# Kernel optimization log

Hardware: AMD Instinct MI355X
Metric: run time of the kernel (lower is better)

## Reference

```python
import jax, jax.numpy as jnp
import numpy as np
import math

B, S, D, H, W = 1, 2048, 512, 8, 64
DK = D // H
NEG = -1e9


def setup_inputs() -> dict:
    rng = jax.random.key(0)
    ks = jax.random.split(rng, 8)
    sc = 0.02
    return {
        "query": jax.random.normal(ks[0], (B, S, D), jnp.float32),
        "key": jax.random.normal(ks[1], (B, S, D), jnp.float32),
        "value": jax.random.normal(ks[2], (B, S, D), jnp.float32),
        "Wq": jax.random.normal(ks[3], (D, D), jnp.float32) * sc,
        "Wk": jax.random.normal(ks[4], (D, D), jnp.float32) * sc,
        "Wv": jax.random.normal(ks[5], (D, D), jnp.float32) * sc,
        "Wo": jax.random.normal(ks[6], (D, D), jnp.float32) * sc,
        "bo": jax.random.normal(ks[7], (D,), jnp.float32) * sc,
    }


def reference(query, key, value, Wq, Wk, Wv, Wo, bo):
    b, s, d = query.shape

    def proj(x, Wm):
        # [B,S,D] -> [B,H,S,DK]
        return (x @ Wm.T).reshape(b, s, H, DK).transpose(0, 2, 1, 3)

    Q = proj(query, Wq)
    K = proj(key, Wk)
    V = proj(value, Wv)

    i = jnp.arange(s)
    rel = jnp.arange(-W, 1)                     # causal band: keys i-W..i
    idx = i[:, None] + rel[None, :]             # [S, W+1]
    valid = idx >= 0
    idxc = jnp.clip(idx, 0, s - 1)

    Kw = K[:, :, idxc, :]                       # [B,H,S,W+1,DK]
    Vw = V[:, :, idxc, :]

    scores = jnp.einsum('bhsd,bhsrd->bhsr', Q, Kw) / math.sqrt(DK)
    decay_bias = 0.1 * jnp.exp(-0.1 * jnp.abs(rel.astype(jnp.float32)))
    scores = jnp.where(valid[None, None], scores + decay_bias, NEG)
    probs = jax.nn.softmax(scores, axis=-1)     # [B,H,S,W+1]

    out = jnp.einsum('bhsr,bhsrd->bhsd', probs, Vw)
    out = out.transpose(0, 2, 1, 3).reshape(b, s, d)
    output = out @ Wo.T + bo

    # attention_weights [B,H,S,2W]: only rows with window_size <= 2W are written
    win = jnp.minimum(s, i + W + 1) - jnp.maximum(0, i - W)   # [S]
    stored = win <= 2 * W
    slot = jnp.arange(2 * W)
    ridx = slot[None, :] + jnp.maximum(W - i, 0)[:, None]     # [S,2W] slot->band index
    vmask = (ridx <= W) & (slot[None, :] < win[:, None]) & stored[:, None]
    gath = jnp.take_along_axis(probs, jnp.clip(ridx, 0, W)[None, None], axis=-1)
    attn_w = jnp.where(vmask[None, None], gath, 0.0)

    return output, attn_w
```

## Files before the change

kernel.cpp:

```cpp
#include <hip/hip_runtime.h>
#include <stdint.h>

#define SEQ   2048
#define DM    512
#define NHEAD 8
#define DKH   64
#define WIN   64
#define NEGV  -1000000000.0f

typedef __attribute__((ext_vector_type(8))) short          short8;
typedef __attribute__((ext_vector_type(4))) float          float4v;
typedef __attribute__((ext_vector_type(8))) unsigned short ushort8v;

__device__ __forceinline__ unsigned short f2bf(float x) {
    uint32_t u = __float_as_uint(x);
    uint32_t r = (u + 0x7FFFu + ((u >> 16) & 1u)) >> 16;
    return (unsigned short)r;
}
__device__ __forceinline__ float bf2f(unsigned short u) {
    return __uint_as_float(((uint32_t)u) << 16);
}

__device__ __forceinline__ void async_cp16(const void* g, void* lds) {
    __builtin_amdgcn_global_load_lds(
        (const __attribute__((address_space(1))) unsigned int*)(uintptr_t)g,
        (__attribute__((address_space(3))) unsigned int*)(uint32_t)(uintptr_t)lds,
        16, 0, 0);
}

__global__ __launch_bounds__(256)
void cast7_kernel(const float* __restrict__ q, const float* __restrict__ k,
                  const float* __restrict__ v, const float* __restrict__ wq,
                  const float* __restrict__ wk, const float* __restrict__ wv,
                  const float* __restrict__ wo, unsigned short* __restrict__ dst)
{
    int g = (blockIdx.x * 256 + threadIdx.x) * 8;
    const float* src; int off;
    if      (g < 1048576) { src = q;  off = g; }
    else if (g < 2097152) { src = k;  off = g - 1048576; }
    else if (g < 3145728) { src = v;  off = g - 2097152; }
    else if (g < 3407872) { src = wq; off = g - 3145728; }
    else if (g < 3670016) { src = wk; off = g - 3407872; }
    else if (g < 3932160) { src = wv; off = g - 3670016; }
    else                  { src = wo; off = g - 3932160; }
    float4 x0 = *(const float4*)(src + off);
    float4 x1 = *(const float4*)(src + off + 4);
    ushort8v o;
    o[0] = f2bf(x0.x); o[1] = f2bf(x0.y); o[2] = f2bf(x0.z); o[3] = f2bf(x0.w);
    o[4] = f2bf(x1.x); o[5] = f2bf(x1.y); o[6] = f2bf(x1.z); o[7] = f2bf(x1.w);
    *(ushort8v*)(dst + g) = o;
}

template<bool BIAS, bool OUT_BF16>
__device__ __forceinline__ void gemm_mfma_body(const unsigned short* __restrict__ A,
                                               const unsigned short* __restrict__ B,
                                               const float* __restrict__ bias,
                                               void* __restrict__ Cv)
{
    __shared__ __align__(16) unsigned short As[128 * 32];
    __shared__ __align__(16) unsigned short Bs[128 * 32];

    const int tid  = threadIdx.x;
    const int m0   = blockIdx.x * 128;
    const int n0   = blockIdx.y * 128;
    const int lane = tid & 63;
    const int wave = tid >> 6;
    const int wm   = (wave >> 1) * 64;
    const int wn   = (wave & 1) * 64;
    const int lm   = lane & 15;
    const int lk   = (lane >> 4) * 8;

    float4v acc[4][4] = {};

    for (int k0 = 0; k0 < 512; k0 += 32) {
        #pragma unroll
        for (int h = 0; h < 2; h++) {
            int c  = tid + h * 256;
            int r  = c >> 2;
            int kc = (c & 3) * 8;
            async_cp16(A + (size_t)(m0 + r) * 512 + k0 + kc, As + c * 8);
            async_cp16(B + (size_t)(n0 + r) * 512 + k0 + kc, Bs + c * 8);
        }
        __syncthreads();

        short8 av[4], bv[4];
        #pragma unroll
        for (int mt = 0; mt < 4; mt++)
            av[mt] = *(const short8*)(As + (wm + mt * 16 + lm) * 32 + lk);
        #pragma unroll
        for (int nt = 0; nt < 4; nt++)
            bv[nt] = *(const short8*)(Bs + (wn + nt * 16 + lm) * 32 + lk);
        #pragma unroll
        for (int mt = 0; mt < 4; mt++)
            #pragma unroll
            for (int nt = 0; nt < 4; nt++)
                acc[mt][nt] = __builtin_amdgcn_mfma_f32_16x16x32_bf16(
                    av[mt], bv[nt], acc[mt][nt], 0, 0, 0);
        __syncthreads();
    }

    const int r0 = (lane >> 4) * 4;
    const int cn = lane & 15;
    #pragma unroll
    for (int nt = 0; nt < 4; nt++) {
        int gcol = n0 + wn + nt * 16 + cn;
        float b = BIAS ? bias[gcol] : 0.f;
        #pragma unroll
        for (int mt = 0; mt < 4; mt++) {
            int grow = m0 + wm + mt * 16 + r0;
            #pragma unroll
            for (int reg = 0; reg < 4; reg++) {
                float val = acc[mt][nt][reg] + b;
                if (OUT_BF16)
                    ((unsigned short*)Cv)[(size_t)(grow + reg) * 512 + gcol] = f2bf(val);
                else
                    ((float*)Cv)[(size_t)(grow + reg) * 512 + gcol] = val;
            }
        }
    }
}

__global__ __launch_bounds__(256)
void qkv_gemm_kernel(const unsigned short* __restrict__ qb,
                     const unsigned short* __restrict__ kb,
                     const unsigned short* __restrict__ vb,
                     const unsigned short* __restrict__ wqb,
                     const unsigned short* __restrict__ wkb,
                     const unsigned short* __restrict__ wvb,
                     unsigned short* __restrict__ Qp, unsigned short* __restrict__ Kp,
                     unsigned short* __restrict__ Vp)
{
    const unsigned short *A, *B; unsigned short* C;
    if (blockIdx.z == 0)      { A = qb; B = wqb; C = Qp; }
    else if (blockIdx.z == 1) { A = kb; B = wkb; C = Kp; }
    else                      { A = vb; B = wvb; C = Vp; }
    gemm_mfma_body<false, true>(A, B, nullptr, C);
}

__global__ __launch_bounds__(256)
void out_gemm_kernel(const unsigned short* __restrict__ ctxb,
                     const unsigned short* __restrict__ wob,
                     const float* __restrict__ bo, float* __restrict__ out)
{
    gemm_mfma_body<true, false>(ctxb, wob, bo, out);
}

#define VTS 152

__global__ __launch_bounds__(256)
void attn_kernel(const unsigned short* __restrict__ Qp,
                 const unsigned short* __restrict__ Kp,
                 const unsigned short* __restrict__ Vp,
                 unsigned short* __restrict__ ctxb,
                 float* __restrict__ attnw)
{
    __shared__ __align__(16) unsigned short Qs[64 * 72];
    __shared__ __align__(16) unsigned short Ks[128 * 72];
    __shared__ __align__(16) unsigned short Vt[64 * VTS];
    __shared__ __align__(16) unsigned short Ps[4][16][96];

    const int h   = blockIdx.y;
    const int q0  = blockIdx.x * 64;
    const int tid = threadIdx.x;

    for (int c = tid; c < 512; c += 256) {
        int row = c >> 3, ch = c & 7;
        *(ushort8v*)&Qs[row * 72 + ch * 8] =
            *(const ushort8v*)&Qp[(size_t)(q0 + row) * 512 + h * 64 + ch * 8];
    }
    for (int c = tid; c < 1024; c += 256) {
        int row = c >> 3, ch = c & 7;
        int g = q0 - 64 + row;
        ushort8v val = {0, 0, 0, 0, 0, 0, 0, 0};
        if (g >= 0)
            val = *(const ushort8v*)&Kp[(size_t)g * 512 + h * 64 + ch * 8];
        *(ushort8v*)&Ks[row * 72 + ch * 8] = val;
    }
    {
        int key = tid >> 1, dh = tid & 1;
        int g = q0 - 64 + key;
        ushort8v vv[4];
        #pragma unroll
        for (int j = 0; j < 4; j++) {
            ushort8v z = {0, 0, 0, 0, 0, 0, 0, 0};
            vv[j] = (g >= 0)
                ? *(const ushort8v*)&Vp[(size_t)g * 512 + h * 64 + dh * 32 + j * 8]
                : z;
        }
        #pragma unroll
        for (int j = 0; j < 4; j++)
            #pragma unroll
            for (int e = 0; e < 8; e++)
                Vt[(dh * 32 + j * 8 + e) * VTS + key] = vv[j][e];
    }
    for (int t = tid; t < 64 * 24; t += 256) {
        int d = t / 24, c = 128 + (t % 24);
        Vt[d * VTS + c] = 0;
    }
    __syncthreads();

    const int lane = tid & 63;
    const int w    = tid >> 6;
    const int lm   = lane & 15;
    const int g16  = lane >> 4;
    const int lk8  = g16 * 8;

    short8 av0 = *(const short8*)&Qs[(w * 16 + lm) * 72 + lk8];
    short8 av1 = *(const short8*)&Qs[(w * 16 + lm) * 72 + 32 + lk8];
    float4v sc[5];
    #pragma unroll
    for (int kt = 0; kt < 5; kt++) {
        const unsigned short* kr = &Ks[(w * 16 + kt * 16 + lm) * 72];
        short8 b0 = *(const short8*)(kr + lk8);
        short8 b1 = *(const short8*)(kr + 32 + lk8);
        float4v a = {0.f, 0.f, 0.f, 0.f};
        a = __builtin_amdgcn_mfma_f32_16x16x32_bf16(av0, b0, a, 0, 0, 0);
        a = __builtin_amdgcn_mfma_f32_16x16x32_bf16(av1, b1, a, 0, 0, 0);
        sc[kt] = a;
    }

    float v[5][4];
    #pragma unroll
    for (int kt = 0; kt < 5; kt++) {
        int kk = kt * 16 + lm;
        int g  = q0 - 64 + w * 16 + kk;
        #pragma unroll
        for (int reg = 0; reg < 4; reg++) {
            int rr = g16 * 4 + reg;
            bool valid = (kk >= rr) && (kk <= rr + 64) && (g >= 0);
            v[kt][reg] = valid
                ? sc[kt][reg] * 0.125f + 0.1f * __expf(-0.1f * (float)(64 + rr - kk))
                : NEGV;
        }
    }

    float mx[4], sm[4];
    #pragma unroll
    for (int reg = 0; reg < 4; reg++) {
        float m = v[0][reg];
        #pragma unroll
        for (int kt = 1; kt < 5; kt++) m = fmaxf(m, v[kt][reg]);
        mx[reg] = m;
    }
    #pragma unroll
    for (int off = 1; off < 16; off <<= 1)
        #pragma unroll
        for (int reg = 0; reg < 4; reg++)
            mx[reg] = fmaxf(mx[reg], __shfl_xor(mx[reg], off));
    float p[5][4];
    #pragma unroll
    for (int reg = 0; reg < 4; reg++) {
        float s = 0.f;
        #pragma unroll
        for (int kt = 0; kt < 5; kt++) {
            float e = __expf(v[kt][reg] - mx[reg]);
            p[kt][reg] = e;
            s += e;
        }
        sm[reg] = s;
    }
    #pragma unroll
    for (int off = 1; off < 16; off <<= 1)
        #pragma unroll
        for (int reg = 0; reg < 4; reg++)
            sm[reg] += __shfl_xor(sm[reg], off);
    #pragma unroll
    for (int reg = 0; reg < 4; reg++) {
        float inv = 1.f / sm[reg];
        #pragma unroll
        for (int kt = 0; kt < 5; kt++) p[kt][reg] *= inv;
    }

    #pragma unroll
    for (int kt = 0; kt < 5; kt++)
        #pragma unroll
        for (int reg = 0; reg < 4; reg++)
            Ps[w][g16 * 4 + reg][kt * 16 + lm] = f2bf(p[kt][reg]);
    #pragma unroll
    for (int reg = 0; reg < 4; reg++)
        Ps[w][g16 * 4 + reg][80 + lm] = 0;

    __syncthreads();

    float4v oacc[4] = {};
    #pragma unroll
    for (int ks = 0; ks < 3; ks++) {
        short8 pa = *(const short8*)&Ps[w][lm][ks * 32 + lk8];
        #pragma unroll
        for (int nt = 0; nt < 4; nt++) {
            short8 vb = *(const short8*)&Vt[(nt * 16 + lm) * VTS + w * 16 + ks * 32 + lk8];
            oacc[nt] = __builtin_amdgcn_mfma_f32_16x16x32_bf16(pa, vb, oacc[nt], 0, 0, 0);
        }
    }

    #pragma unroll
    for (int nt = 0; nt < 4; nt++)
        #pragma unroll
        for (int reg = 0; reg < 4; reg++) {
            int i = q0 + w * 16 + g16 * 4 + reg;
            ctxb[(size_t)i * 512 + h * 64 + nt * 16 + lm] = f2bf(oacc[nt][reg]);
        }

    __syncthreads();

    for (int t = tid; t < 64 * 128; t += 256) {
        int ql = t >> 7, slot = t & 127;
        int i  = q0 + ql;
        float val = 0.f;
        if (q0 == 0) {
            if (slot <= ql) {
                int kk = (ql & 15) + slot + 64 - ql;
                val = bf2f(Ps[ql >> 4][ql & 15][kk]);
            }
        } else if (q0 == SEQ - 64) {
            if (slot <= 64) {
                int kk = (ql & 15) + slot;
                val = bf2f(Ps[ql >> 4][ql & 15][kk]);
            }
        }
        attnw[((size_t)h * SEQ + i) * 2 * WIN + slot] = val;
    }
}

extern "C" void kernel_launch(void* const* d_in, const int* in_sizes, int n_in,
                              void* d_out, int out_size, void* d_ws, size_t ws_size,
                              hipStream_t stream)
{
    const float* query = (const float*)d_in[0];
    const float* key   = (const float*)d_in[1];
    const float* value = (const float*)d_in[2];
    const float* Wq    = (const float*)d_in[3];
    const float* Wk    = (const float*)d_in[4];
    const float* Wv    = (const float*)d_in[5];
    const float* Wo    = (const float*)d_in[6];
    const float* bo    = (const float*)d_in[7];

    float* out   = (float*)d_out;
    float* attnw = out + SEQ * DM;

    unsigned short* qb   = (unsigned short*)d_ws;
    unsigned short* kb   = qb  + 1048576;
    unsigned short* vb   = kb  + 1048576;
    unsigned short* wqb  = vb  + 1048576;
    unsigned short* wkb  = wqb + 262144;
    unsigned short* wvb  = wkb + 262144;
    unsigned short* wob  = wvb + 262144;
    unsigned short* Qp   = wob + 262144;
    unsigned short* Kp   = Qp  + 1048576;
    unsigned short* Vp   = Kp  + 1048576;
    unsigned short* ctxb = Vp  + 1048576;

    cast7_kernel<<<2048, 256, 0, stream>>>(query, key, value, Wq, Wk, Wv, Wo, qb);

    dim3 g1(SEQ / 128, DM / 128, 3);
    qkv_gemm_kernel<<<g1, 256, 0, stream>>>(qb, kb, vb, wqb, wkb, wvb, Qp, Kp, Vp);

    dim3 g2(SEQ / 64, NHEAD);
    attn_kernel<<<g2, 256, 0, stream>>>(Qp, Kp, Vp, ctxb, attnw);

    dim3 g3(SEQ / 128, DM / 128);
    out_gemm_kernel<<<g3, 256, 0, stream>>>(ctxb, wob, bo, out);
}
```

Before: 114.6 us.

## Double-buffer LDS tiles in bf16 MFMA GEMM to overlap loads with compute

The GEMM k-loop now uses two LDS buffers for the A and B tiles. It issues the async global-to-LDS copies for the next k-slice before running the MFMAs on the current one, so memory latency can overlap with math. LDS use per block doubles to 32KB, which may reduce occupancy. Correctness depends on the single barrier per iteration draining the async loads (vmcnt) before the next read.

```diff
diff --git a/kernel.cpp b/kernel.cpp
--- a/kernel.cpp
+++ b/kernel.cpp
@@ -57,8 +57,8 @@
                                                const float* __restrict__ bias,
                                                void* __restrict__ Cv)
 {
-    __shared__ __align__(16) unsigned short As[128 * 32];
-    __shared__ __align__(16) unsigned short Bs[128 * 32];
+    __shared__ __align__(16) unsigned short As[2][128 * 32];
+    __shared__ __align__(16) unsigned short Bs[2][128 * 32];
 
     const int tid  = threadIdx.x;
     const int m0   = blockIdx.x * 128;
@@ -72,30 +72,44 @@
 
     float4v acc[4][4] = {};
 
-    for (int k0 = 0; k0 < 512; k0 += 32) {
-        #pragma unroll
-        for (int h = 0; h < 2; h++) {
-            int c  = tid + h * 256;
-            int r  = c >> 2;
-            int kc = (c & 3) * 8;
-            async_cp16(A + (size_t)(m0 + r) * 512 + k0 + kc, As + c * 8);
-            async_cp16(B + (size_t)(n0 + r) * 512 + k0 + kc, Bs + c * 8);
-        }
-        __syncthreads();
+    #pragma unroll
+    for (int h = 0; h < 2; h++) {
+        int c  = tid + h * 256;
+        int rr = c >> 2;
+        int kk = (c & 3) * 8;
+        async_cp16(A + (size_t)(m0 + rr) * 512 + kk, &As[0][c * 8]);
+        async_cp16(B + (size_t)(n0 + rr) * 512 + kk, &Bs[0][c * 8]);
+    }
+    __syncthreads();
+
+    for (int t = 0; t < 16; ++t) {
+        const int cur = t & 1;
+        if (t < 15) {
+            const int k0 = (t + 1) * 32;
+            #pragma unroll
+            for (int h = 0; h < 2; h++) {
+                int c  = tid + h * 256;
+                int rr = c >> 2;
+                int kk = (c & 3) * 8;
+                async_cp16(A + (size_t)(m0 + rr) * 512 + k0 + kk, &As[cur ^ 1][c * 8]);
+                async_cp16(B + (size_t)(n0 + rr) * 512 + k0 + kk, &Bs[cur ^ 1][c * 8]);
+            }
+        }
 
         short8 av[4], bv[4];
         #pragma unroll
         for (int mt = 0; mt < 4; mt++)
-            av[mt] = *(const short8*)(As + (wm + mt * 16 + lm) * 32 + lk);
+            av[mt] = *(const short8*)(&As[cur][(wm + mt * 16 + lm) * 32 + lk]);
         #pragma unroll
         for (int nt = 0; nt < 4; nt++)
-            bv[nt] = *(const short8*)(Bs + (wn + nt * 16 + lm) * 32 + lk);
+            bv[nt] = *(const short8*)(&Bs[cur][(wn + nt * 16 + lm) * 32 + lk]);
         #pragma unroll
         for (int mt = 0; mt < 4; mt++)
             #pragma unroll
             for (int nt = 0; nt < 4; nt++)
                 acc[mt][nt] = __builtin_amdgcn_mfma_f32_16x16x32_bf16(
                     av[mt], bv[nt], acc[mt][nt], 0, 0, 0);
+
         __syncthreads();
     }
 
```

Result: faster. 109.6 us (-4.3%).
